# Performance work log

Hardware: AMD Instinct MI355X
Metric: run time of the kernel (lower is better)

Reference implementation:

```python
import jax, jax.numpy as jnp
import numpy as np

KH, KW = 3, 3
STRIDE = (1, 1)
PAD = ((1, 1), (1, 1))
WEIGHT_BIT = 8


def asym_quant_params(num_bits, smin, smax):
    # ZeroQ asymmetric_linear_quantization_params (signed, integral zero point)
    n = 2.0 ** num_bits - 1.0
    scale = n / jnp.maximum(smax - smin, 1e-8)
    zero_point = jnp.round(scale * smin) + 2.0 ** (num_bits - 1)
    return scale, zero_point


def setup_inputs() -> dict:
    key = jax.random.key(0)
    k1, k2, k3 = jax.random.split(key, 3)
    x = jax.random.normal(k1, (16, 128, 56, 56), dtype=jnp.float32)
    weight = jax.random.normal(k2, (128, 128, 3, 3), dtype=jnp.float32) * 0.05
    bias = jax.random.normal(k3, (128,), dtype=jnp.float32) * 0.1
    return {"x": x, "weight": weight, "bias": bias, "activation_bit": 8}


def reference(x, weight, bias, activation_bit):
    B, C, H, W = x.shape
    Cout = weight.shape[0]

    # nn.functional.unfold(x, 3, stride=1, padding=1).transpose(1, 2)
    # conv_general_dilated_patches emits feature dim ordered (c, kh, kw),
    # matching torch unfold's channel-major layout.
    patches = jax.lax.conv_general_dilated_patches(
        x, filter_shape=(KH, KW), window_strides=STRIDE, padding=PAD)
    _, F, OH, OW = patches.shape          # F = C*KH*KW
    L = OH * OW
    calc_x = patches.reshape(B, F, L).transpose(0, 2, 1)  # [B, L, F]

    # ----- weight quantization: per-output-channel asymmetric int8 -----
    w2 = weight.reshape(Cout, -1)                          # [Cout, F]
    w_min = w2.min(axis=1)
    w_max = w2.max(axis=1)
    scale_w, zp_w = asym_quant_params(WEIGHT_BIT, w_min, w_max)  # [Cout]
    nw = 2.0 ** (WEIGHT_BIT - 1)
    qw = jnp.clip(jnp.round(scale_w[:, None] * w2 - zp_w[:, None]), -nw, nw - 1)

    # ----- activation quantization: per-tensor asymmetric -----
    x_min = calc_x.min()
    x_max = calc_x.max()
    scale_x, zp_x = asym_quant_params(activation_bit, x_min, x_max)
    nx = 2.0 ** (activation_bit - 1)
    qx = jnp.clip(jnp.round(scale_x * calc_x - zp_x), -nx, nx - 1)  # [B, L, F]

    # bias: linear_quantize(bias, scale_w*scale_x, 0)
    qb = jnp.round(scale_w * scale_x * bias)                # [Cout]

    # integer matmul + asymmetric zero-point correction
    # real value r ~= (q + zp) / scale, so
    # x.w*sx*sw = qx.qw + zp_w*sum(qx) + zp_x*sum(qw) + K*zp_w*zp_x
    mult_res = jnp.einsum('blf,of->blo', qx, qw)            # [B, L, Cout]
    K = w2.shape[1]
    res = (mult_res
           + zp_w * qx.sum(-1, keepdims=True)               # [B, L, 1]*[Cout]
           + zp_x * qw.sum(axis=1)                          # [Cout]
           + K * zp_w * zp_x
           + qb)                                            # [B, L, Cout]

    # requantize accumulator to activation_bit bits, then dequantize
    r_min, r_max = res.min(), res.max()
    scale_r, zp_r = asym_quant_params(activation_bit, r_min, r_max)
    nr = 2.0 ** (activation_bit - 1)
    qr = jnp.clip(jnp.round(scale_r * res - zp_r), -nr, nr - 1)
    out = (qr + zp_r) / scale_r / (scale_w * scale_x)       # [B, L, Cout]

    return out.transpose(0, 2, 1)                           # [B, Cout, L]
```

## Files before the change

### kernel.cpp

```cpp
#include <hip/hip_runtime.h>
#include <stdint.h>

#pragma clang fp contract(off)

typedef __attribute__((ext_vector_type(4))) int i32x4;
typedef __attribute__((ext_vector_type(16))) int i32x16;

#define B_    16
#define C_    128
#define HW_   56
#define L_    3136
#define CO_   128
#define F_    1152
#define M_    50176
#define NT_   784

#define OFF_PBMIN 0
#define OFF_PBMAX 3136
#define OFF_PRMIN 6272
#define OFF_PRMAX 9408
#define OFF_SW    12544
#define OFF_ZPW   13056
#define OFF_SXZX  13568
#define OFF_CNT   14080
#define OFF_QS    15616
#define OFF_QW    16384
#define OFF_QX    163840
#define OFF_S     6586368
#define OFF_RES   6787072

__device__ __forceinline__ int read_abit(const int* p) {
    int i = *p;
    if (i > 0 && i < 32) return i;
    float f = __int_as_float(i);
    int fi = (int)f;
    return (fi > 0 && fi < 32) ? fi : 8;
}

__device__ __forceinline__ int swz_tile(int blk) {
    return (blk & 7) * 98 + (blk >> 3);
}

__device__ __forceinline__ void gsync(char* ws, int sp) {
    unsigned* base = (unsigned*)(ws + OFF_CNT) + sp * 128;
    __syncthreads();
    if (threadIdx.x == 0) {
        __threadfence();
        atomicAdd(&base[(blockIdx.x & 7) * 16], 1u);
    }
    if (threadIdx.x < 8) {
        while (__hip_atomic_load(&base[threadIdx.x * 16],
                                 __ATOMIC_RELAXED, __HIP_MEMORY_SCOPE_AGENT) < 98u)
            __builtin_amdgcn_s_sleep(2);
    }
    __threadfence();
    __syncthreads();
}

__device__ __forceinline__ void block_fminmax(float& mn, float& mx, float* sred) {
    for (int m = 32; m; m >>= 1) {
        mn = fminf(mn, __shfl_xor(mn, m));
        mx = fmaxf(mx, __shfl_xor(mx, m));
    }
    int w = threadIdx.x >> 6;
    if ((threadIdx.x & 63) == 0) { sred[w] = mn; sred[4 + w] = mx; }
    __syncthreads();
    mn = fminf(fminf(sred[0], sred[1]), fminf(sred[2], sred[3]));
    mx = fmaxf(fmaxf(sred[4], sred[5]), fmaxf(sred[6], sred[7]));
    __syncthreads();
}
__device__ __forceinline__ void block_iminmax(int& mn, int& mx, int* ired) {
    for (int m = 32; m; m >>= 1) {
        mn = min(mn, __shfl_xor(mn, m));
        mx = max(mx, __shfl_xor(mx, m));
    }
    int w = threadIdx.x >> 6;
    if ((threadIdx.x & 63) == 0) { ired[w] = mn; ired[4 + w] = mx; }
    __syncthreads();
    mn = min(min(ired[0], ired[1]), min(ired[2], ired[3]));
    mx = max(max(ired[4], ired[5]), max(ired[6], ired[7]));
    __syncthreads();
}
__device__ __forceinline__ int block_isum(int v, int* ired) {
    for (int m = 32; m; m >>= 1) v += __shfl_xor(v, m);
    int w = threadIdx.x >> 6;
    if ((threadIdx.x & 63) == 0) ired[w] = v;
    __syncthreads();
    v = ired[0] + ired[1] + ired[2] + ired[3];
    __syncthreads();
    return v;
}

__global__ __launch_bounds__(256) void kA1(const float4* __restrict__ x4,
                                           char* __restrict__ ws) {
    __shared__ float sred[8];
    float mn = 0.0f, mx = 0.0f;
    int base = blockIdx.x * blockDim.x + threadIdx.x;
    int stride = NT_ * 256;
    #pragma unroll
    for (int k = 0; k < 8; ++k) {
        float4 v = x4[base + k * stride];
        mn = fminf(mn, fminf(fminf(v.x, v.y), fminf(v.z, v.w)));
        mx = fmaxf(mx, fmaxf(fmaxf(v.x, v.y), fmaxf(v.z, v.w)));
    }
    block_fminmax(mn, mx, sred);
    if (threadIdx.x == 0) {
        ((float*)(ws + OFF_PBMIN))[blockIdx.x] = mn;
        ((float*)(ws + OFF_PBMAX))[blockIdx.x] = mx;
    }
}

__global__ __launch_bounds__(256) void kA2(const float* __restrict__ wgt,
                                           const int* __restrict__ abit_p,
                                           char* __restrict__ ws) {
    __shared__ float sred[8];
    __shared__ int ired[8];
    if (blockIdx.x == CO_) {
        const float* pbmin = (const float*)(ws + OFF_PBMIN);
        const float* pbmax = (const float*)(ws + OFF_PBMAX);
        float mn = 0.0f, mx = 0.0f;
        for (int i = threadIdx.x; i < NT_; i += 256) {
            mn = fminf(mn, pbmin[i]);
            mx = fmaxf(mx, pbmax[i]);
        }
        block_fminmax(mn, mx, sred);
        if (threadIdx.x == 0) {
            int abit = read_abit(abit_p);
            float nlv = (float)((1 << abit) - 1);
            float sx = nlv / fmaxf(mx - mn, 1e-8f);
            float zx = rintf(sx * mn) + (float)(1 << (abit - 1));
            ((float*)(ws + OFF_SXZX))[0] = sx;
            ((float*)(ws + OFF_SXZX))[1] = zx;
        }
        return;
    }
    int o = blockIdx.x;
    const float* wr = wgt + o * F_;
    float mn = 3.4e38f, mx = -3.4e38f;
    for (int f = threadIdx.x; f < F_; f += 256) {
        float v = wr[f];
        mn = fminf(mn, v); mx = fmaxf(mx, v);
    }
    block_fminmax(mn, mx, sred);
    float sw = 255.0f / fmaxf(mx - mn, 1e-8f);
    float zw = rintf(sw * mn) + 128.0f;
    signed char* qw = (signed char*)(ws + OFF_QW);
    int qsum = 0;
    for (int f = threadIdx.x; f < F_; f += 256) {
        float q = fminf(fmaxf(rintf(sw * wr[f] - zw), -128.0f), 127.0f);
        int qi = (int)q;
        qsum += qi;
        int c = f / 9, j = f - c * 9;
        qw[j * 16384 + (c >> 4) * 2048 + (o << 4) + (c & 15)] = (signed char)qi;
    }
    qsum = block_isum(qsum, ired);
    if (threadIdx.x == 0) {
        ((int*)(ws + OFF_QS))[o]  = qsum;
        ((int*)(ws + OFF_ZPW))[o] = (int)zw;
        ((float*)(ws + OFF_SW))[o] = sw;
    }
}

__device__ __forceinline__ void dev_p2x(const float* __restrict__ x, char* ws, char* pool,
                                        float sx, float zx, int nx) {
    int (*ssum)[64] = (int(*)[64])pool;
    float lo = -(float)nx, hif = (float)(nx - 1);
    signed char* qxt = (signed char*)(ws + OFF_QX);
    int gid = swz_tile(blockIdx.x);
    int b = gid / 49, lcq = gid - b * 49;
    int l0 = lcq * 64;
    int t = threadIdx.x, lane = t & 63, cgp = t >> 6;
    int l = l0 + lane;
    const float* xb = x + ((size_t)b * C_) * L_ + l;
    int4* dst = (int4*)(qxt + ((size_t)(b * L_ + l)) * 128);
    int psum = 0;
    #pragma unroll
    for (int ii = 0; ii < 2; ++ii) {
        int c16 = (cgp + 4 * ii) * 16;
        int wds[4];
        #pragma unroll
        for (int k = 0; k < 4; ++k) {
            int wv = 0;
            #pragma unroll
            for (int e = 0; e < 4; ++e) {
                int c = c16 + 4 * k + e;
                float v = xb[(size_t)c * L_];
                int qi = (int)fminf(fmaxf(rintf(sx * v - zx), lo), hif);
                psum += qi;
                wv |= (qi & 255) << (8 * e);
            }
            wds[k] = wv;
        }
        int4 vv; vv.x = wds[0]; vv.y = wds[1]; vv.z = wds[2]; vv.w = wds[3];
        dst[c16 >> 4] = vv;
    }
    ssum[cgp][lane] = psum;
    __syncthreads();
    if (cgp == 0) {
        int* S = (int*)(ws + OFF_S);
        S[b * L_ + l] = ssum[0][lane] + ssum[1][lane] + ssum[2][lane] + ssum[3][lane];
    }
    __syncthreads();
}

template <bool WRITE_RES>
__device__ __forceinline__ void dev_p3(char* __restrict__ ws, char* pool, int* ired,
                                       const float* __restrict__ bias,
                                       int abit, float sx, float zx,
                                       i32x16& acc0, i32x16& acc1) {
    signed char* As = (signed char*)pool;
    signed char* Bs = (signed char*)(pool + 8192);
    int* S_s = (int*)(pool + 24576);
    int* sq  = (int*)(pool + 25504);
    const signed char* qxt = (const signed char*)(ws + OFF_QX);
    const signed char* qw  = (const signed char*)(ws + OFF_QW);
    const int* Sg  = (const int*)(ws + OFF_S);
    const int* zpw = (const int*)(ws + OFF_ZPW);

    int t = threadIdx.x;
    int mg = swz_tile(blockIdx.x) * 64;
    int b = mg / L_, l0 = mg - b * L_;
    int prow0 = l0 / HW_;
    int nx = 1 << (abit - 1);
    int q0 = min(max(-(int)zx, -nx), nx - 1);
    int pw = (q0 & 255) * 0x01010101;
    int4 pad4; pad4.x = pw; pad4.y = pw; pad4.z = pw; pad4.w = pw;
    int padS = C_ * q0;
    const signed char* qxtb = qxt + (size_t)b * L_ * 128;
    const int* Sb = Sg + b * L_;

    int chA = t & 7, rowA0 = t >> 3, rowA1 = rowA0 + 32;
    int li0 = l0 + rowA0, li1 = l0 + rowA1;
    int oh0 = li0 / HW_, ow0 = li0 - oh0 * HW_;
    int oh1 = li1 / HW_, ow1 = li1 - oh1 * HW_;

    int4 a0, a1, br0, br1, br2, br3;
    #define P3_LOAD_A(J) do {                                                          \
        int kh = (J) / 3 - 1, kw = (J) % 3 - 1;                                        \
        int ih = oh0 + kh, iw = ow0 + kw;                                              \
        a0 = ((unsigned)ih < HW_ && (unsigned)iw < HW_)                                \
             ? *(const int4*)(qxtb + ((ih * HW_ + iw) << 7) + (chA << 4)) : pad4;      \
        ih = oh1 + kh; iw = ow1 + kw;                                                  \
        a1 = ((unsigned)ih < HW_ && (unsigned)iw < HW_)                                \
             ? *(const int4*)(qxtb + ((ih * HW_ + iw) << 7) + (chA << 4)) : pad4;      \
    } while (0)
    #define P3_LOAD_B(J) do {                                                          \
        const int4* src = (const int4*)(qw + (J) * 16384);                             \
        br0 = src[t]; br1 = src[256 + t]; br2 = src[512 + t]; br3 = src[768 + t];      \
    } while (0)

    P3_LOAD_A(0); P3_LOAD_B(0);
    if (t < 232) {
        int ri = t / 58, c1 = t - ri * 58;
        int ih = prow0 - 1 + ri, iw = c1 - 1;
        S_s[t] = ((unsigned)ih < HW_ && (unsigned)iw < HW_) ? Sb[ih * HW_ + iw] : padS;
    }
    __syncthreads();
    if (t < 64) {
        int l = l0 + t;
        int oh = l / HW_, ow = l - oh * HW_;
        int ri = oh - prow0 + 1, ci = ow + 1;
        int s = 0;
        #pragma unroll
        for (int dr = -1; dr <= 1; ++dr)
            #pragma unroll
            for (int dc = -1; dc <= 1; ++dc)
                s += S_s[(ri + dr) * 58 + ci + dc];
        sq[t] = s;
    }

    int lane = t & 63, w = t >> 6;
    int wm = (w >> 1) << 5, wn = (w & 1) << 6;
    int r = lane & 31, hi = lane >> 5;
    #pragma unroll
    for (int i = 0; i < 16; ++i) { acc0[i] = 0; acc1[i] = 0; }

    #pragma unroll
    for (int j = 0; j < 9; ++j) {
        if (j > 0) __syncthreads();
        *(int4*)&As[(rowA0 << 7) + ((chA ^ (rowA0 & 7)) << 4)] = a0;
        *(int4*)&As[(rowA1 << 7) + ((chA ^ (rowA1 & 7)) << 4)] = a1;
        {
            int4* d = (int4*)Bs;
            d[t] = br0; d[256 + t] = br1; d[512 + t] = br2; d[768 + t] = br3;
        }
        if (j < 8) { P3_LOAD_A(j + 1); P3_LOAD_B(j + 1); }
        __syncthreads();
        i32x4 af[4], bf0[4], bf1[4];
        #pragma unroll
        for (int kk = 0; kk < 4; ++kk) {
            int ch2 = kk * 2 + hi, row = wm + r;
            af[kk]  = *(const i32x4*)&As[(row << 7) + ((ch2 ^ (row & 7)) << 4)];
            bf0[kk] = *(const i32x4*)&Bs[ch2 * 2048 + ((wn + r) << 4)];
            bf1[kk] = *(const i32x4*)&Bs[ch2 * 2048 + ((wn + 32 + r) << 4)];
        }
        #pragma unroll
        for (int kk = 0; kk < 4; ++kk) {
            acc0 = __builtin_amdgcn_mfma_i32_32x32x32_i8(af[kk], bf0[kk], acc0, 0, 0, 0);
            acc1 = __builtin_amdgcn_mfma_i32_32x32x32_i8(af[kk], bf1[kk], acc1, 0, 0, 0);
        }
    }
    #undef P3_LOAD_A
    #undef P3_LOAD_B

    int o0 = wn + r, o1 = wn + 32 + r;
    const int* qs = (const int*)(ws + OFF_QS);
    const float* swp = (const float*)(ws + OFF_SW);
    int zxi = (int)zx;
    int zw0 = zpw[o0], zw1 = zpw[o1];
    int c0 = zxi * qs[o0] + F_ * zw0 * zxi + (int)rintf(swp[o0] * sx * bias[o0]);
    int c1 = zxi * qs[o1] + F_ * zw1 * zxi + (int)rintf(swp[o1] * sx * bias[o1]);
    int lmin = INT32_MAX, lmax = INT32_MIN;
    int* resp = (int*)(ws + OFF_RES);
    #pragma unroll
    for (int g = 0; g < 16; ++g) {
        int row = wm + (g & 3) + ((g >> 2) << 3) + (hi << 2);
        int s = sq[row];
        int v0 = acc0[g] + zw0 * s + c0;
        int v1 = acc1[g] + zw1 * s + c1;
        acc0[g] = v0; acc1[g] = v1;
        lmin = min(lmin, min(v0, v1));
        lmax = max(lmax, max(v0, v1));
        if (WRITE_RES) {
            int m = mg + row;
            resp[m * CO_ + o0] = v0;
            resp[m * CO_ + o1] = v1;
        }
    }
    block_iminmax(lmin, lmax, ired);
    if (t == 0) {
        ((int*)(ws + OFF_PRMIN))[blockIdx.x] = lmin;
        ((int*)(ws + OFF_PRMAX))[blockIdx.x] = lmax;
    }
    __syncthreads();
}

__device__ __forceinline__ void dev_reduce_pr(const char* ws, int* ired,
                                              int& rmin, int& rmax) {
    const int* prmin = (const int*)(ws + OFF_PRMIN);
    const int* prmax = (const int*)(ws + OFF_PRMAX);
    int mn = INT32_MAX, mx = INT32_MIN;
    for (int i = threadIdx.x; i < NT_; i += 256) {
        mn = min(mn, prmin[i]);
        mx = max(mx, prmax[i]);
    }
    block_iminmax(mn, mx, ired);
    rmin = mn; rmax = mx;
}

__device__ __forceinline__ void dev_p4(const char* ws, char* pool, float* __restrict__ out,
                                       int abit, float sx, int rmin, int rmax,
                                       const i32x16& acc0, const i32x16& acc1) {
    const float* scale_w = (const float*)(ws + OFF_SW);
    float* tile = (float*)pool;
    int t = threadIdx.x;
    int mg = swz_tile(blockIdx.x) * 64;
    int b = mg / L_, l0 = mg - b * L_;
    int lane = t & 63, w = t >> 6;
    int wm = (w >> 1) << 5, wn = (w & 1) << 6;
    int r = lane & 31, hi = lane >> 5;
    int o0 = wn + r, o1 = wn + 32 + r;
    int nx = 1 << (abit - 1);
    float nlev = (float)((1 << abit) - 1);
    float rminf = (float)rmin, rmaxf = (float)rmax;
    float sr = nlev / fmaxf(rmaxf - rminf, 1e-8f);
    float zr = rintf(sr * rminf) + (float)nx;
    float lo = -(float)nx, hiq = (float)(nx - 1);
    float swsx0 = scale_w[o0] * sx, swsx1 = scale_w[o1] * sx;
    #pragma unroll
    for (int g = 0; g < 16; ++g) {
        int row = wm + (g & 3) + ((g >> 2) << 3) + (hi << 2);
        float qa = fminf(fmaxf(rintf(sr * (float)acc0[g] - zr), lo), hiq);
        float qb = fminf(fmaxf(rintf(sr * (float)acc1[g] - zr), lo), hiq);
        tile[row * 129 + o0] = ((qa + zr) / sr) / swsx0;
        tile[row * 129 + o1] = ((qb + zr) / sr) / swsx1;
    }
    __syncthreads();
    #pragma unroll
    for (int i = 0; i < 8; ++i) {
        int o = (t >> 4) + i * 16;
        int l4 = (t & 15) * 4;
        float4 f;
        #pragma unroll
        for (int jj = 0; jj < 4; ++jj)
            ((float*)&f)[jj] = tile[(l4 + jj) * 129 + o];
        *(float4*)(out + ((size_t)(b * CO_ + o)) * L_ + l0 + l4) = f;
    }
}

__global__ __launch_bounds__(256, 4) void kB(const float* __restrict__ x,
                                             const float* __restrict__ bias,
                                             const int* __restrict__ abit_p,
                                             char* __restrict__ ws,
                                             float* __restrict__ out) {
    __shared__ __align__(16) char pool[33280];
    __shared__ int ired[8];

    float sx = ((const float*)(ws + OFF_SXZX))[0];
    float zx = ((const float*)(ws + OFF_SXZX))[1];
    int abit = read_abit(abit_p);
    int nx = 1 << (abit - 1);

    dev_p2x(x, ws, pool, sx, zx, nx);
    gsync(ws, 0);

    i32x16 acc0, acc1;
    dev_p3<false>(ws, pool, ired, bias, abit, sx, zx, acc0, acc1);
    gsync(ws, 1);

    int rmin, rmax;
    dev_reduce_pr(ws, ired, rmin, rmax);
    dev_p4(ws, pool, out, abit, sx, rmin, rmax, acc0, acc1);
}

__global__ __launch_bounds__(256) void fbB1(const float* __restrict__ x,
                                            const int* __restrict__ abit_p,
                                            char* __restrict__ ws) {
    __shared__ __align__(16) char pool[1024];
    float sx = ((const float*)(ws + OFF_SXZX))[0];
    float zx = ((const float*)(ws + OFF_SXZX))[1];
    int abit = read_abit(abit_p);
    int nx = 1 << (abit - 1);
    dev_p2x(x, ws, pool, sx, zx, nx);
}

__global__ __launch_bounds__(256, 4) void fbB2(const float* __restrict__ bias,
                                               const int* __restrict__ abit_p,
                                               char* __restrict__ ws) {
    __shared__ __align__(16) char pool[25760];
    __shared__ int ired[8];
    float sx = ((const float*)(ws + OFF_SXZX))[0];
    float zx = ((const float*)(ws + OFF_SXZX))[1];
    int abit = read_abit(abit_p);
    i32x16 acc0, acc1;
    dev_p3<true>(ws, pool, ired, bias, abit, sx, zx, acc0, acc1);
}

__global__ __launch_bounds__(256) void fbB3(const int* __restrict__ abit_p,
                                            char* __restrict__ ws,
                                            float* __restrict__ out) {
    __shared__ int tile[64 * 65];
    __shared__ int ired[8];
    float sxv = ((const float*)(ws + OFF_SXZX))[0];
    int abit = read_abit(abit_p);
    float nlv = (float)((1 << abit) - 1);
    int rmin, rmax;
    dev_reduce_pr(ws, ired, rmin, rmax);

    const int* res = (const int*)(ws + OFF_RES);
    const float* scale_w = (const float*)(ws + OFF_SW);
    int t = threadIdx.x;
    int bid = blockIdx.x;
    int lcq = bid % 49; int tmp2 = bid / 49; int ocq = tmp2 & 1; int b = tmp2 >> 1;
    int l0 = lcq * 64, o0 = ocq * 64;

    const int* resb = res + ((size_t)(b * L_ + l0)) * CO_ + o0;
    #pragma unroll
    for (int i = 0; i < 4; ++i) {
        int lr = (t >> 4) + i * 16;
        int oc4 = (t & 15) * 4;
        int4 v = *(const int4*)(resb + lr * CO_ + oc4);
        int* d = &tile[lr * 65 + oc4];
        d[0] = v.x; d[1] = v.y; d[2] = v.z; d[3] = v.w;
    }
    int nxq = 1 << (abit - 1);
    float rminf = (float)rmin, rmaxf = (float)rmax;
    float sr = nlv / fmaxf(rmaxf - rminf, 1e-8f);
    float zr = rintf(sr * rminf) + (float)nxq;
    float lo = -(float)nxq, hiq = (float)(nxq - 1);
    __syncthreads();
    #pragma unroll
    for (int i = 0; i < 4; ++i) {
        int o = (t >> 4) + i * 16;
        int l4 = (t & 15) * 4;
        float swsx = scale_w[o0 + o] * sxv;
        float4 f;
        #pragma unroll
        for (int jj = 0; jj < 4; ++jj) {
            int rv = tile[(l4 + jj) * 65 + o];
            float q = fminf(fmaxf(rintf(sr * (float)rv - zr), lo), hiq);
            ((float*)&f)[jj] = ((q + zr) / sr) / swsx;
        }
        *(float4*)(out + ((size_t)(b * CO_ + o0 + o)) * L_ + l0 + l4) = f;
    }
}


extern "C" void kernel_launch(void* const* d_in, const int* in_sizes, int n_in,
                              void* d_out, int out_size, void* d_ws, size_t ws_size,
                              hipStream_t stream) {
    const float* x      = (const float*)d_in[0];
    const float* weight = (const float*)d_in[1];
    const float* bias   = (const float*)d_in[2];
    const int*   abit   = (const int*)d_in[3];
    float* out = (float*)d_out;
    char* ws = (char*)d_ws;

    int dev = 0;
    hipGetDevice(&dev);
    int ncu = 0;
    hipDeviceGetAttribute(&ncu, hipDeviceAttributeMultiprocessorCount, dev);
    int nb = 0;
    hipOccupancyMaxActiveBlocksPerMultiprocessor(&nb, (const void*)kB, 256, 0);

    kA1<<<NT_, 256, 0, stream>>>((const float4*)x, ws);
    kA2<<<CO_ + 1, 256, 0, stream>>>(weight, abit, ws);

    if (nb > 0 && (long)nb * (long)ncu >= NT_) {
        hipMemsetAsync(ws + OFF_CNT, 0, 1024, stream);
        kB<<<NT_, 256, 0, stream>>>(x, bias, abit, ws, out);
    } else {
        fbB1<<<NT_, 256, 0, stream>>>(x, abit, ws);
        fbB2<<<NT_, 256, 0, stream>>>(bias, abit, ws);
        fbB3<<<1568, 256, 0, stream>>>(abit, ws, out);
    }
}
```

Measured before the change: 54.63 us.

## Fuse activation quantization into conv GEMM via in-LDS halo tile, drop one grid sync

Removes the separate quantize-and-store pass for activations. Each block now loads a 4-row input halo straight from x, quantizes it into a swizzled LDS buffer, and computes the row sums locally. The tile grows to 112 output pixels (two image rows) with four MFMA accumulators per wave, and weight tiles are double-buffered so each tap needs only one barrier. The grid drops to 448 blocks with one global barrier instead of two, cutting the int8 activation round trip through global memory. In exchange, blocks use more LDS and registers with lower occupancy, halo rows are re-quantized by neighbouring blocks, and some lanes go partly idle on the 112-row tile.

```diff
diff --git a/kernel.cpp b/kernel.cpp
--- a/kernel.cpp
+++ b/kernel.cpp
@@ -13,21 +13,24 @@
 #define CO_   128
 #define F_    1152
 #define M_    50176
-#define NT_   784
-
-#define OFF_PBMIN 0
-#define OFF_PBMAX 3136
-#define OFF_PRMIN 6272
-#define OFF_PRMAX 9408
-#define OFF_SW    12544
-#define OFF_ZPW   13056
-#define OFF_SXZX  13568
-#define OFF_CNT   14080
-#define OFF_QS    15616
+#define NT1_  784
+#define NTC_  448
+
+#define OFF_PRMIN 0
+#define OFF_PRMAX 2048
+#define OFF_PBMIN 4096
+#define OFF_PBMAX 8192
+#define OFF_SW    12288
+#define OFF_ZPW   12800
+#define OFF_SXZX  13312
+#define OFF_CNT   13440
+#define OFF_QS    14080
 #define OFF_QW    16384
-#define OFF_QX    163840
-#define OFF_S     6586368
-#define OFF_RES   6787072
+#define OFF_RES   163840
+
+#define HALO_B 29696
+#define BS_B   16384
+#define POOL_B (HALO_B + 2 * BS_B)
 
 __device__ __forceinline__ int read_abit(const int* p) {
     int i = *p;
@@ -38,11 +41,11 @@
 }
 
 __device__ __forceinline__ int swz_tile(int blk) {
-    return (blk & 7) * 98 + (blk >> 3);
-}
-
-__device__ __forceinline__ void gsync(char* ws, int sp) {
-    unsigned* base = (unsigned*)(ws + OFF_CNT) + sp * 128;
+    return (blk & 7) * 56 + (blk >> 3);
+}
+
+__device__ __forceinline__ void gsync(char* ws) {
+    unsigned* base = (unsigned*)(ws + OFF_CNT);
     __syncthreads();
     if (threadIdx.x == 0) {
         __threadfence();
@@ -50,7 +53,7 @@
     }
     if (threadIdx.x < 8) {
         while (__hip_atomic_load(&base[threadIdx.x * 16],
-                                 __ATOMIC_RELAXED, __HIP_MEMORY_SCOPE_AGENT) < 98u)
+                                 __ATOMIC_RELAXED, __HIP_MEMORY_SCOPE_AGENT) < 56u)
             __builtin_amdgcn_s_sleep(2);
     }
     __threadfence();
@@ -96,7 +99,7 @@
     __shared__ float sred[8];
     float mn = 0.0f, mx = 0.0f;
     int base = blockIdx.x * blockDim.x + threadIdx.x;
-    int stride = NT_ * 256;
+    int stride = NT1_ * 256;
     #pragma unroll
     for (int k = 0; k < 8; ++k) {
         float4 v = x4[base + k * stride];
@@ -119,7 +122,7 @@
         const float* pbmin = (const float*)(ws + OFF_PBMIN);
         const float* pbmax = (const float*)(ws + OFF_PBMAX);
         float mn = 0.0f, mx = 0.0f;
-        for (int i = threadIdx.x; i < NT_; i += 256) {
+        for (int i = threadIdx.x; i < NT1_; i += 256) {
             mn = fminf(mn, pbmin[i]);
             mx = fmaxf(mx, pbmax[i]);
         }
@@ -161,103 +164,92 @@
     }
 }
 
-__device__ __forceinline__ void dev_p2x(const float* __restrict__ x, char* ws, char* pool,
-                                        float sx, float zx, int nx) {
-    int (*ssum)[64] = (int(*)[64])pool;
-    float lo = -(float)nx, hif = (float)(nx - 1);
-    signed char* qxt = (signed char*)(ws + OFF_QX);
-    int gid = swz_tile(blockIdx.x);
-    int b = gid / 49, lcq = gid - b * 49;
-    int l0 = lcq * 64;
-    int t = threadIdx.x, lane = t & 63, cgp = t >> 6;
-    int l = l0 + lane;
-    const float* xb = x + ((size_t)b * C_) * L_ + l;
-    int4* dst = (int4*)(qxt + ((size_t)(b * L_ + l)) * 128);
-    int psum = 0;
-    #pragma unroll
-    for (int ii = 0; ii < 2; ++ii) {
-        int c16 = (cgp + 4 * ii) * 16;
-        int wds[4];
-        #pragma unroll
-        for (int k = 0; k < 4; ++k) {
-            int wv = 0;
-            #pragma unroll
-            for (int e = 0; e < 4; ++e) {
-                int c = c16 + 4 * k + e;
-                float v = xb[(size_t)c * L_];
-                int qi = (int)fminf(fmaxf(rintf(sx * v - zx), lo), hif);
-                psum += qi;
-                wv |= (qi & 255) << (8 * e);
-            }
-            wds[k] = wv;
-        }
-        int4 vv; vv.x = wds[0]; vv.y = wds[1]; vv.z = wds[2]; vv.w = wds[3];
-        dst[c16 >> 4] = vv;
-    }
-    ssum[cgp][lane] = psum;
-    __syncthreads();
-    if (cgp == 0) {
-        int* S = (int*)(ws + OFF_S);
-        S[b * L_ + l] = ssum[0][lane] + ssum[1][lane] + ssum[2][lane] + ssum[3][lane];
-    }
-    __syncthreads();
-}
-
 template <bool WRITE_RES>
-__device__ __forceinline__ void dev_p3(char* __restrict__ ws, char* pool, int* ired,
-                                       const float* __restrict__ bias,
-                                       int abit, float sx, float zx,
-                                       i32x16& acc0, i32x16& acc1) {
-    signed char* As = (signed char*)pool;
-    signed char* Bs = (signed char*)(pool + 8192);
-    int* S_s = (int*)(pool + 24576);
-    int* sq  = (int*)(pool + 25504);
-    const signed char* qxt = (const signed char*)(ws + OFF_QX);
-    const signed char* qw  = (const signed char*)(ws + OFF_QW);
-    const int* Sg  = (const int*)(ws + OFF_S);
+__device__ __forceinline__ void dev_main(const float* __restrict__ x,
+                                         const float* __restrict__ bias,
+                                         char* __restrict__ ws, char* pool,
+                                         int* S_s, int* sq, int* ired,
+                                         int abit, float sx, float zx,
+                                         i32x16& a00, i32x16& a01,
+                                         i32x16& a10, i32x16& a11,
+                                         int& mgout) {
+    signed char* NB  = (signed char*)pool;
+    signed char* Bs0 = (signed char*)(pool + HALO_B);
+    signed char* Bs1 = Bs0 + BS_B;
+    const signed char* qw = (const signed char*)(ws + OFF_QW);
     const int* zpw = (const int*)(ws + OFF_ZPW);
 
     int t = threadIdx.x;
-    int mg = swz_tile(blockIdx.x) * 64;
+    int mg = swz_tile(blockIdx.x) * 112;
+    mgout = mg;
     int b = mg / L_, l0 = mg - b * L_;
     int prow0 = l0 / HW_;
     int nx = 1 << (abit - 1);
     int q0 = min(max(-(int)zx, -nx), nx - 1);
     int pw = (q0 & 255) * 0x01010101;
     int4 pad4; pad4.x = pw; pad4.y = pw; pad4.z = pw; pad4.w = pw;
-    int padS = C_ * q0;
-    const signed char* qxtb = qxt + (size_t)b * L_ * 128;
-    const int* Sb = Sg + b * L_;
-
-    int chA = t & 7, rowA0 = t >> 3, rowA1 = rowA0 + 32;
-    int li0 = l0 + rowA0, li1 = l0 + rowA1;
-    int oh0 = li0 / HW_, ow0 = li0 - oh0 * HW_;
-    int oh1 = li1 / HW_, ow1 = li1 - oh1 * HW_;
-
-    int4 a0, a1, br0, br1, br2, br3;
-    #define P3_LOAD_A(J) do {                                                          \
-        int kh = (J) / 3 - 1, kw = (J) % 3 - 1;                                        \
-        int ih = oh0 + kh, iw = ow0 + kw;                                              \
-        a0 = ((unsigned)ih < HW_ && (unsigned)iw < HW_)                                \
-             ? *(const int4*)(qxtb + ((ih * HW_ + iw) << 7) + (chA << 4)) : pad4;      \
-        ih = oh1 + kh; iw = ow1 + kw;                                                  \
-        a1 = ((unsigned)ih < HW_ && (unsigned)iw < HW_)                                \
-             ? *(const int4*)(qxtb + ((ih * HW_ + iw) << 7) + (chA << 4)) : pad4;      \
-    } while (0)
-    #define P3_LOAD_B(J) do {                                                          \
-        const int4* src = (const int4*)(qw + (J) * 16384);                             \
-        br0 = src[t]; br1 = src[256 + t]; br2 = src[512 + t]; br3 = src[768 + t];      \
-    } while (0)
-
-    P3_LOAD_A(0); P3_LOAD_B(0);
+    const float* xb = x + (size_t)b * C_ * L_;
+
+    int4 br0, br1, br2, br3;
+    {
+        const int4* src = (const int4*)qw;
+        br0 = src[t]; br1 = src[256 + t]; br2 = src[512 + t]; br3 = src[768 + t];
+    }
+
+    #pragma unroll
+    for (int i = 0; i < 8; ++i) {
+        int s = t + i * 256;
+        if (s < 1856) ((int4*)NB)[s] = pad4;
+    }
+    __syncthreads();
+
+    {
+        float lo = -(float)nx, hif = (float)(nx - 1);
+        #pragma unroll
+        for (int i = 0; i < 28; ++i) {
+            int u = t + i * 256;
+            int c = u / 56, rem = u - c * 56;
+            int ri = rem / 14, f4 = rem - ri * 14;
+            int ih = prow0 - 1 + ri;
+            if ((unsigned)ih < HW_) {
+                float4 v = *(const float4*)(xb + (size_t)c * L_ + ih * HW_ + f4 * 4);
+                int ch = c >> 4, byte = c & 15;
+                #pragma unroll
+                for (int k = 0; k < 4; ++k) {
+                    float xv = ((const float*)&v)[k];
+                    int qi = (int)fminf(fmaxf(rintf(sx * xv - zx), lo), hif);
+                    int pix = ri * 58 + f4 * 4 + k + 1;
+                    NB[(pix << 7) + ((ch ^ (pix & 7)) << 4) + byte] = (signed char)qi;
+                }
+            }
+        }
+    }
+    {
+        int4* d = (int4*)Bs0;
+        d[t] = br0; d[256 + t] = br1; d[512 + t] = br2; d[768 + t] = br3;
+        const int4* src = (const int4*)(qw + BS_B);
+        br0 = src[t]; br1 = src[256 + t]; br2 = src[512 + t]; br3 = src[768 + t];
+    }
+    __syncthreads();
+
     if (t < 232) {
-        int ri = t / 58, c1 = t - ri * 58;
-        int ih = prow0 - 1 + ri, iw = c1 - 1;
-        S_s[t] = ((unsigned)ih < HW_ && (unsigned)iw < HW_) ? Sb[ih * HW_ + iw] : padS;
-    }
-    __syncthreads();
-    if (t < 64) {
-        int l = l0 + t;
+        int s = 0;
+        #pragma unroll
+        for (int ch = 0; ch < 8; ++ch) {
+            int4 v = *(const int4*)&NB[(t << 7) + ((ch ^ (t & 7)) << 4)];
+            #pragma unroll
+            for (int k2 = 0; k2 < 4; ++k2) {
+                int wv = ((const int*)&v)[k2];
+                s += (int)(signed char)wv + (int)(signed char)(wv >> 8)
+                   + (int)(signed char)(wv >> 16) + (int)(signed char)(wv >> 24);
+            }
+        }
+        S_s[t] = s;
+    }
+    __syncthreads();
+    if (t < 128) {
+        int rl = min(t, 111);
+        int l = l0 + rl;
         int oh = l / HW_, ow = l - oh * HW_;
         int ri = oh - prow0 + 1, ci = ow + 1;
         int s = 0;
@@ -270,38 +262,57 @@
     }
 
     int lane = t & 63, w = t >> 6;
-    int wm = (w >> 1) << 5, wn = (w & 1) << 6;
+    int wm = (w >> 1) << 6;
+    int wn = (w & 1) << 6;
     int r = lane & 31, hi = lane >> 5;
-    #pragma unroll
-    for (int i = 0; i < 16; ++i) { acc0[i] = 0; acc1[i] = 0; }
+
+    int pb0, pb1;
+    {
+        int l = l0 + wm + r;
+        int oh = l / HW_, ow = l - oh * HW_;
+        pb0 = (oh - prow0 + 1) * 58 + ow + 1;
+    }
+    {
+        int rl = min(wm + 32 + r, 111);
+        int l = l0 + rl;
+        int oh = l / HW_, ow = l - oh * HW_;
+        pb1 = (oh - prow0 + 1) * 58 + ow + 1;
+    }
+
+    #pragma unroll
+    for (int i = 0; i < 16; ++i) { a00[i] = 0; a01[i] = 0; a10[i] = 0; a11[i] = 0; }
 
     #pragma unroll
     for (int j = 0; j < 9; ++j) {
-        if (j > 0) __syncthreads();
-        *(int4*)&As[(rowA0 << 7) + ((chA ^ (rowA0 & 7)) << 4)] = a0;
-        *(int4*)&As[(rowA1 << 7) + ((chA ^ (rowA1 & 7)) << 4)] = a1;
-        {
-            int4* d = (int4*)Bs;
+        if (j < 8) {
+            int4* d = (int4*)(((j + 1) & 1) ? Bs1 : Bs0);
             d[t] = br0; d[256 + t] = br1; d[512 + t] = br2; d[768 + t] = br3;
-        }
-        if (j < 8) { P3_LOAD_A(j + 1); P3_LOAD_B(j + 1); }
+            if (j < 7) {
+                const int4* src = (const int4*)(qw + (j + 2) * BS_B);
+                br0 = src[t]; br1 = src[256 + t]; br2 = src[512 + t]; br3 = src[768 + t];
+            }
+        }
+        const signed char* Bc = (j & 1) ? Bs1 : Bs0;
+        int dj = (j / 3 - 1) * 58 + (j % 3 - 1);
+        i32x4 af0[4], af1[4], bf0[4], bf1[4];
+        #pragma unroll
+        for (int kk = 0; kk < 4; ++kk) {
+            int ch2 = kk * 2 + hi;
+            int p0 = pb0 + dj, p1 = pb1 + dj;
+            af0[kk] = *(const i32x4*)&NB[(p0 << 7) + ((ch2 ^ (p0 & 7)) << 4)];
+            af1[kk] = *(const i32x4*)&NB[(p1 << 7) + ((ch2 ^ (p1 & 7)) << 4)];
+            bf0[kk] = *(const i32x4*)&Bc[ch2 * 2048 + ((wn + r) << 4)];
+            bf1[kk] = *(const i32x4*)&Bc[ch2 * 2048 + ((wn + 32 + r) << 4)];
+        }
+        #pragma unroll
+        for (int kk = 0; kk < 4; ++kk) {
+            a00 = __builtin_amdgcn_mfma_i32_32x32x32_i8(af0[kk], bf0[kk], a00, 0, 0, 0);
+            a01 = __builtin_amdgcn_mfma_i32_32x32x32_i8(af0[kk], bf1[kk], a01, 0, 0, 0);
+            a10 = __builtin_amdgcn_mfma_i32_32x32x32_i8(af1[kk], bf0[kk], a10, 0, 0, 0);
+            a11 = __builtin_amdgcn_mfma_i32_32x32x32_i8(af1[kk], bf1[kk], a11, 0, 0, 0);
+        }
         __syncthreads();
-        i32x4 af[4], bf0[4], bf1[4];
-        #pragma unroll
-        for (int kk = 0; kk < 4; ++kk) {
-            int ch2 = kk * 2 + hi, row = wm + r;
-            af[kk]  = *(const i32x4*)&As[(row << 7) + ((ch2 ^ (row & 7)) << 4)];
-            bf0[kk] = *(const i32x4*)&Bs[ch2 * 2048 + ((wn + r) << 4)];
-            bf1[kk] = *(const i32x4*)&Bs[ch2 * 2048 + ((wn + 32 + r) << 4)];
-        }
-        #pragma unroll
-        for (int kk = 0; kk < 4; ++kk) {
-            acc0 = __builtin_amdgcn_mfma_i32_32x32x32_i8(af[kk], bf0[kk], acc0, 0, 0, 0);
-            acc1 = __builtin_amdgcn_mfma_i32_32x32x32_i8(af[kk], bf1[kk], acc1, 0, 0, 0);
-        }
-    }
-    #undef P3_LOAD_A
-    #undef P3_LOAD_B
+    }
 
     int o0 = wn + r, o1 = wn + 32 + r;
     const int* qs = (const int*)(ws + OFF_QS);
@@ -314,17 +325,27 @@
     int* resp = (int*)(ws + OFF_RES);
     #pragma unroll
     for (int g = 0; g < 16; ++g) {
-        int row = wm + (g & 3) + ((g >> 2) << 3) + (hi << 2);
-        int s = sq[row];
-        int v0 = acc0[g] + zw0 * s + c0;
-        int v1 = acc1[g] + zw1 * s + c1;
-        acc0[g] = v0; acc1[g] = v1;
-        lmin = min(lmin, min(v0, v1));
-        lmax = max(lmax, max(v0, v1));
+        int sub = (g & 3) + ((g >> 2) << 3) + (hi << 2);
+        int r0 = wm + sub, r1 = wm + 32 + sub;
+        int s0 = sq[r0], s1 = sq[r1];
+        int v00 = a00[g] + zw0 * s0 + c0;
+        int v01 = a01[g] + zw1 * s0 + c1;
+        int v10 = a10[g] + zw0 * s1 + c0;
+        int v11 = a11[g] + zw1 * s1 + c1;
+        a00[g] = v00; a01[g] = v01; a10[g] = v10; a11[g] = v11;
+        lmin = min(lmin, min(v00, v01));
+        lmax = max(lmax, max(v00, v01));
+        if (r1 < 112) {
+            lmin = min(lmin, min(v10, v11));
+            lmax = max(lmax, max(v10, v11));
+        }
         if (WRITE_RES) {
-            int m = mg + row;
-            resp[m * CO_ + o0] = v0;
-            resp[m * CO_ + o1] = v1;
+            resp[(mg + r0) * CO_ + o0] = v00;
+            resp[(mg + r0) * CO_ + o1] = v01;
+            if (r1 < 112) {
+                resp[(mg + r1) * CO_ + o0] = v10;
+                resp[(mg + r1) * CO_ + o1] = v11;
+            }
         }
     }
     block_iminmax(lmin, lmax, ired);
@@ -340,7 +361,7 @@
     const int* prmin = (const int*)(ws + OFF_PRMIN);
     const int* prmax = (const int*)(ws + OFF_PRMAX);
     int mn = INT32_MAX, mx = INT32_MIN;
-    for (int i = threadIdx.x; i < NT_; i += 256) {
+    for (int i = threadIdx.x; i < NTC_; i += 256) {
         mn = min(mn, prmin[i]);
         mx = max(mx, prmax[i]);
     }
@@ -348,97 +369,98 @@
     rmin = mn; rmax = mx;
 }
 
-__device__ __forceinline__ void dev_p4(const char* ws, char* pool, float* __restrict__ out,
-                                       int abit, float sx, int rmin, int rmax,
-                                       const i32x16& acc0, const i32x16& acc1) {
-    const float* scale_w = (const float*)(ws + OFF_SW);
-    float* tile = (float*)pool;
+__global__ __launch_bounds__(256, 2) void kC(const float* __restrict__ x,
+                                             const float* __restrict__ bias,
+                                             const int* __restrict__ abit_p,
+                                             char* __restrict__ ws,
+                                             float* __restrict__ out) {
+    __shared__ __align__(16) char pool[POOL_B];
+    __shared__ int S_s[232];
+    __shared__ int sq[128];
+    __shared__ int ired[8];
+
+    float sx = ((const float*)(ws + OFF_SXZX))[0];
+    float zx = ((const float*)(ws + OFF_SXZX))[1];
+    int abit = read_abit(abit_p);
+
+    i32x16 a00, a01, a10, a11;
+    int mg;
+    dev_main<false>(x, bias, ws, pool, S_s, sq, ired, abit, sx, zx,
+                    a00, a01, a10, a11, mg);
+    gsync(ws);
+
+    int rmin, rmax;
+    dev_reduce_pr(ws, ired, rmin, rmax);
+
+    const float* swp = (const float*)(ws + OFF_SW);
     int t = threadIdx.x;
-    int mg = swz_tile(blockIdx.x) * 64;
     int b = mg / L_, l0 = mg - b * L_;
     int lane = t & 63, w = t >> 6;
-    int wm = (w >> 1) << 5, wn = (w & 1) << 6;
+    int wm = (w >> 1) << 6, wn = (w & 1) << 6;
     int r = lane & 31, hi = lane >> 5;
     int o0 = wn + r, o1 = wn + 32 + r;
     int nx = 1 << (abit - 1);
     float nlev = (float)((1 << abit) - 1);
-    float rminf = (float)rmin, rmaxf = (float)rmax;
-    float sr = nlev / fmaxf(rmaxf - rminf, 1e-8f);
-    float zr = rintf(sr * rminf) + (float)nx;
+    float sr = nlev / fmaxf((float)rmax - (float)rmin, 1e-8f);
+    float zr = rintf(sr * (float)rmin) + (float)nx;
     float lo = -(float)nx, hiq = (float)(nx - 1);
-    float swsx0 = scale_w[o0] * sx, swsx1 = scale_w[o1] * sx;
-    #pragma unroll
-    for (int g = 0; g < 16; ++g) {
-        int row = wm + (g & 3) + ((g >> 2) << 3) + (hi << 2);
-        float qa = fminf(fmaxf(rintf(sr * (float)acc0[g] - zr), lo), hiq);
-        float qb = fminf(fmaxf(rintf(sr * (float)acc1[g] - zr), lo), hiq);
-        tile[row * 129 + o0] = ((qa + zr) / sr) / swsx0;
-        tile[row * 129 + o1] = ((qb + zr) / sr) / swsx1;
-    }
-    __syncthreads();
-    #pragma unroll
-    for (int i = 0; i < 8; ++i) {
-        int o = (t >> 4) + i * 16;
-        int l4 = (t & 15) * 4;
-        float4 f;
-        #pragma unroll
-        for (int jj = 0; jj < 4; ++jj)
-            ((float*)&f)[jj] = tile[(l4 + jj) * 129 + o];
-        *(float4*)(out + ((size_t)(b * CO_ + o)) * L_ + l0 + l4) = f;
-    }
-}
-
-__global__ __launch_bounds__(256, 4) void kB(const float* __restrict__ x,
-                                             const float* __restrict__ bias,
-                                             const int* __restrict__ abit_p,
-                                             char* __restrict__ ws,
-                                             float* __restrict__ out) {
-    __shared__ __align__(16) char pool[33280];
-    __shared__ int ired[8];
-
-    float sx = ((const float*)(ws + OFF_SXZX))[0];
-    float zx = ((const float*)(ws + OFF_SXZX))[1];
-    int abit = read_abit(abit_p);
-    int nx = 1 << (abit - 1);
-
-    dev_p2x(x, ws, pool, sx, zx, nx);
-    gsync(ws, 0);
-
-    i32x16 acc0, acc1;
-    dev_p3<false>(ws, pool, ired, bias, abit, sx, zx, acc0, acc1);
-    gsync(ws, 1);
-
-    int rmin, rmax;
-    dev_reduce_pr(ws, ired, rmin, rmax);
-    dev_p4(ws, pool, out, abit, sx, rmin, rmax, acc0, acc1);
-}
-
-__global__ __launch_bounds__(256) void fbB1(const float* __restrict__ x,
-                                            const int* __restrict__ abit_p,
-                                            char* __restrict__ ws) {
-    __shared__ __align__(16) char pool[1024];
-    float sx = ((const float*)(ws + OFF_SXZX))[0];
-    float zx = ((const float*)(ws + OFF_SXZX))[1];
-    int abit = read_abit(abit_p);
-    int nx = 1 << (abit - 1);
-    dev_p2x(x, ws, pool, sx, zx, nx);
-}
-
-__global__ __launch_bounds__(256, 4) void fbB2(const float* __restrict__ bias,
-                                               const int* __restrict__ abit_p,
-                                               char* __restrict__ ws) {
-    __shared__ __align__(16) char pool[25760];
+    float swsx0 = swp[o0] * sx, swsx1 = swp[o1] * sx;
+    float* tile = (float*)pool;
+
+    #pragma unroll
+    for (int rid = 0; rid < 2; ++rid) {
+        __syncthreads();
+        if (wm == rid * 64) {
+            #pragma unroll
+            for (int g = 0; g < 16; ++g) {
+                int sub = (g & 3) + ((g >> 2) << 3) + (hi << 2);
+                float qa = fminf(fmaxf(rintf(sr * (float)a00[g] - zr), lo), hiq);
+                float qb = fminf(fmaxf(rintf(sr * (float)a01[g] - zr), lo), hiq);
+                float qc = fminf(fmaxf(rintf(sr * (float)a10[g] - zr), lo), hiq);
+                float qd = fminf(fmaxf(rintf(sr * (float)a11[g] - zr), lo), hiq);
+                tile[sub * 129 + o0] = ((qa + zr) / sr) / swsx0;
+                tile[sub * 129 + o1] = ((qb + zr) / sr) / swsx1;
+                tile[(32 + sub) * 129 + o0] = ((qc + zr) / sr) / swsx0;
+                tile[(32 + sub) * 129 + o1] = ((qd + zr) / sr) / swsx1;
+            }
+        }
+        __syncthreads();
+        int nrows = (rid == 0) ? 64 : 48;
+        #pragma unroll
+        for (int i = 0; i < 8; ++i) {
+            int o = (t >> 4) + i * 16;
+            int l4 = (t & 15) * 4;
+            if (l4 < nrows) {
+                float4 f;
+                #pragma unroll
+                for (int jj = 0; jj < 4; ++jj)
+                    ((float*)&f)[jj] = tile[(l4 + jj) * 129 + o];
+                *(float4*)(out + ((size_t)(b * CO_ + o)) * L_ + l0 + rid * 64 + l4) = f;
+            }
+        }
+    }
+}
+
+__global__ __launch_bounds__(256, 2) void fbC(const float* __restrict__ x,
+                                              const float* __restrict__ bias,
+                                              const int* __restrict__ abit_p,
+                                              char* __restrict__ ws) {
+    __shared__ __align__(16) char pool[POOL_B];
+    __shared__ int S_s[232];
+    __shared__ int sq[128];
     __shared__ int ired[8];
     float sx = ((const float*)(ws + OFF_SXZX))[0];
     float zx = ((const float*)(ws + OFF_SXZX))[1];
     int abit = read_abit(abit_p);
-    i32x16 acc0, acc1;
-    dev_p3<true>(ws, pool, ired, bias, abit, sx, zx, acc0, acc1);
-}
-
-__global__ __launch_bounds__(256) void fbB3(const int* __restrict__ abit_p,
-                                            char* __restrict__ ws,
-                                            float* __restrict__ out) {
+    i32x16 a00, a01, a10, a11;
+    int mg;
+    dev_main<true>(x, bias, ws, pool, S_s, sq, ired, abit, sx, zx,
+                   a00, a01, a10, a11, mg);
+}
+
+__global__ __launch_bounds__(256) void fbD(const int* __restrict__ abit_p,
+                                           char* __restrict__ ws,
+                                           float* __restrict__ out) {
     __shared__ int tile[64 * 65];
     __shared__ int ired[8];
     float sxv = ((const float*)(ws + OFF_SXZX))[0];
@@ -464,9 +486,8 @@
         d[0] = v.x; d[1] = v.y; d[2] = v.z; d[3] = v.w;
     }
     int nxq = 1 << (abit - 1);
-    float rminf = (float)rmin, rmaxf = (float)rmax;
-    float sr = nlv / fmaxf(rmaxf - rminf, 1e-8f);
-    float zr = rintf(sr * rminf) + (float)nxq;
+    float sr = nlv / fmaxf((float)rmax - (float)rmin, 1e-8f);
+    float zr = rintf(sr * (float)rmin) + (float)nxq;
     float lo = -(float)nxq, hiq = (float)(nxq - 1);
     __syncthreads();
     #pragma unroll
@@ -501,17 +522,16 @@
     int ncu = 0;
     hipDeviceGetAttribute(&ncu, hipDeviceAttributeMultiprocessorCount, dev);
     int nb = 0;
-    hipOccupancyMaxActiveBlocksPerMultiprocessor(&nb, (const void*)kB, 256, 0);
-
-    kA1<<<NT_, 256, 0, stream>>>((const float4*)x, ws);
+    hipOccupancyMaxActiveBlocksPerMultiprocessor(&nb, (const void*)kC, 256, 0);
+
+    kA1<<<NT1_, 256, 0, stream>>>((const float4*)x, ws);
     kA2<<<CO_ + 1, 256, 0, stream>>>(weight, abit, ws);
 
-    if (nb > 0 && (long)nb * (long)ncu >= NT_) {
-        hipMemsetAsync(ws + OFF_CNT, 0, 1024, stream);
-        kB<<<NT_, 256, 0, stream>>>(x, bias, abit, ws, out);
+    if (nb > 0 && (long)nb * (long)ncu >= NTC_) {
+        hipMemsetAsync(ws + OFF_CNT, 0, 512, stream);
+        kC<<<NTC_, 256, 0, stream>>>(x, bias, abit, ws, out);
     } else {
-        fbB1<<<NT_, 256, 0, stream>>>(x, abit, ws);
-        fbB2<<<NT_, 256, 0, stream>>>(bias, abit, ws);
-        fbB3<<<1568, 256, 0, stream>>>(abit, ws, out);
-    }
-}
+        fbC<<<NTC_, 256, 0, stream>>>(x, bias, abit, ws);
+        fbD<<<1568, 256, 0, stream>>>(abit, ws, out);
+    }
+}
```

Measured after the change: 95.19 us. 74.2% more time.

## Replace persistent grid-synced kernel with three separate kernel launches

Applied to the files above, without the earlier changes.

Removes the cooperative single-kernel path, which used software grid barriers via atomic counters and kept accumulators in registers across phases. The work is now always split into three kernels: quantize/pack activations, integer GEMM that writes the full int32 result to workspace, and a dequantize kernel that reads it back. This drops the spin-wait barriers, the counter memset and the host-side occupancy queries. In exchange it adds a global write and read of the int32 result tensor and two extra kernel launches.

```diff
diff --git a/kernel.cpp b/kernel.cpp
--- a/kernel.cpp
+++ b/kernel.cpp
@@ -16,18 +16,17 @@
 #define NT_   784
 
 #define OFF_PBMIN 0
-#define OFF_PBMAX 3136
-#define OFF_PRMIN 6272
-#define OFF_PRMAX 9408
-#define OFF_SW    12544
-#define OFF_ZPW   13056
-#define OFF_SXZX  13568
-#define OFF_CNT   14080
-#define OFF_QS    15616
-#define OFF_QW    16384
-#define OFF_QX    163840
-#define OFF_S     6586368
-#define OFF_RES   6787072
+#define OFF_PBMAX 4096
+#define OFF_PRMIN 8192
+#define OFF_PRMAX 12288
+#define OFF_SW    16384
+#define OFF_ZPW   16896
+#define OFF_SXZX  17408
+#define OFF_QS    17536
+#define OFF_QW    18432
+#define OFF_QX    165888
+#define OFF_S     6588416
+#define OFF_RES   6789120
 
 __device__ __forceinline__ int read_abit(const int* p) {
     int i = *p;
@@ -39,22 +38,6 @@
 
 __device__ __forceinline__ int swz_tile(int blk) {
     return (blk & 7) * 98 + (blk >> 3);
-}
-
-__device__ __forceinline__ void gsync(char* ws, int sp) {
-    unsigned* base = (unsigned*)(ws + OFF_CNT) + sp * 128;
-    __syncthreads();
-    if (threadIdx.x == 0) {
-        __threadfence();
-        atomicAdd(&base[(blockIdx.x & 7) * 16], 1u);
-    }
-    if (threadIdx.x < 8) {
-        while (__hip_atomic_load(&base[threadIdx.x * 16],
-                                 __ATOMIC_RELAXED, __HIP_MEMORY_SCOPE_AGENT) < 98u)
-            __builtin_amdgcn_s_sleep(2);
-    }
-    __threadfence();
-    __syncthreads();
 }
 
 __device__ __forceinline__ void block_fminmax(float& mn, float& mx, float* sred) {
@@ -161,9 +144,14 @@
     }
 }
 
-__device__ __forceinline__ void dev_p2x(const float* __restrict__ x, char* ws, char* pool,
-                                        float sx, float zx, int nx) {
-    int (*ssum)[64] = (int(*)[64])pool;
+__global__ __launch_bounds__(256) void kP2x(const float* __restrict__ x,
+                                            const int* __restrict__ abit_p,
+                                            char* __restrict__ ws) {
+    __shared__ int ssum[4][64];
+    float sx = ((const float*)(ws + OFF_SXZX))[0];
+    float zx = ((const float*)(ws + OFF_SXZX))[1];
+    int abit = read_abit(abit_p);
+    int nx = 1 << (abit - 1);
     float lo = -(float)nx, hif = (float)(nx - 1);
     signed char* qxt = (signed char*)(ws + OFF_QX);
     int gid = swz_tile(blockIdx.x);
@@ -200,14 +188,14 @@
         int* S = (int*)(ws + OFF_S);
         S[b * L_ + l] = ssum[0][lane] + ssum[1][lane] + ssum[2][lane] + ssum[3][lane];
     }
-    __syncthreads();
-}
-
-template <bool WRITE_RES>
-__device__ __forceinline__ void dev_p3(char* __restrict__ ws, char* pool, int* ired,
-                                       const float* __restrict__ bias,
-                                       int abit, float sx, float zx,
-                                       i32x16& acc0, i32x16& acc1) {
+}
+
+__global__ __launch_bounds__(256, 4) void kGEMM(const float* __restrict__ bias,
+                                                const int* __restrict__ abit_p,
+                                                char* __restrict__ ws) {
+    __shared__ __align__(16) char pool[25760];
+    __shared__ int ired[8];
+
     signed char* As = (signed char*)pool;
     signed char* Bs = (signed char*)(pool + 8192);
     int* S_s = (int*)(pool + 24576);
@@ -216,6 +204,10 @@
     const signed char* qw  = (const signed char*)(ws + OFF_QW);
     const int* Sg  = (const int*)(ws + OFF_S);
     const int* zpw = (const int*)(ws + OFF_ZPW);
+
+    float sx = ((const float*)(ws + OFF_SXZX))[0];
+    float zx = ((const float*)(ws + OFF_SXZX))[1];
+    int abit = read_abit(abit_p);
 
     int t = threadIdx.x;
     int mg = swz_tile(blockIdx.x) * 64;
@@ -272,6 +264,7 @@
     int lane = t & 63, w = t >> 6;
     int wm = (w >> 1) << 5, wn = (w & 1) << 6;
     int r = lane & 31, hi = lane >> 5;
+    i32x16 acc0, acc1;
     #pragma unroll
     for (int i = 0; i < 16; ++i) { acc0[i] = 0; acc1[i] = 0; }
 
@@ -318,125 +311,20 @@
         int s = sq[row];
         int v0 = acc0[g] + zw0 * s + c0;
         int v1 = acc1[g] + zw1 * s + c1;
-        acc0[g] = v0; acc1[g] = v1;
         lmin = min(lmin, min(v0, v1));
         lmax = max(lmax, max(v0, v1));
-        if (WRITE_RES) {
-            int m = mg + row;
-            resp[m * CO_ + o0] = v0;
-            resp[m * CO_ + o1] = v1;
-        }
+        int m = mg + row;
+        resp[m * CO_ + o0] = v0;
+        resp[m * CO_ + o1] = v1;
     }
     block_iminmax(lmin, lmax, ired);
     if (t == 0) {
         ((int*)(ws + OFF_PRMIN))[blockIdx.x] = lmin;
         ((int*)(ws + OFF_PRMAX))[blockIdx.x] = lmax;
     }
-    __syncthreads();
-}
-
-__device__ __forceinline__ void dev_reduce_pr(const char* ws, int* ired,
-                                              int& rmin, int& rmax) {
-    const int* prmin = (const int*)(ws + OFF_PRMIN);
-    const int* prmax = (const int*)(ws + OFF_PRMAX);
-    int mn = INT32_MAX, mx = INT32_MIN;
-    for (int i = threadIdx.x; i < NT_; i += 256) {
-        mn = min(mn, prmin[i]);
-        mx = max(mx, prmax[i]);
-    }
-    block_iminmax(mn, mx, ired);
-    rmin = mn; rmax = mx;
-}
-
-__device__ __forceinline__ void dev_p4(const char* ws, char* pool, float* __restrict__ out,
-                                       int abit, float sx, int rmin, int rmax,
-                                       const i32x16& acc0, const i32x16& acc1) {
-    const float* scale_w = (const float*)(ws + OFF_SW);
-    float* tile = (float*)pool;
-    int t = threadIdx.x;
-    int mg = swz_tile(blockIdx.x) * 64;
-    int b = mg / L_, l0 = mg - b * L_;
-    int lane = t & 63, w = t >> 6;
-    int wm = (w >> 1) << 5, wn = (w & 1) << 6;
-    int r = lane & 31, hi = lane >> 5;
-    int o0 = wn + r, o1 = wn + 32 + r;
-    int nx = 1 << (abit - 1);
-    float nlev = (float)((1 << abit) - 1);
-    float rminf = (float)rmin, rmaxf = (float)rmax;
-    float sr = nlev / fmaxf(rmaxf - rminf, 1e-8f);
-    float zr = rintf(sr * rminf) + (float)nx;
-    float lo = -(float)nx, hiq = (float)(nx - 1);
-    float swsx0 = scale_w[o0] * sx, swsx1 = scale_w[o1] * sx;
-    #pragma unroll
-    for (int g = 0; g < 16; ++g) {
-        int row = wm + (g & 3) + ((g >> 2) << 3) + (hi << 2);
-        float qa = fminf(fmaxf(rintf(sr * (float)acc0[g] - zr), lo), hiq);
-        float qb = fminf(fmaxf(rintf(sr * (float)acc1[g] - zr), lo), hiq);
-        tile[row * 129 + o0] = ((qa + zr) / sr) / swsx0;
-        tile[row * 129 + o1] = ((qb + zr) / sr) / swsx1;
-    }
-    __syncthreads();
-    #pragma unroll
-    for (int i = 0; i < 8; ++i) {
-        int o = (t >> 4) + i * 16;
-        int l4 = (t & 15) * 4;
-        float4 f;
-        #pragma unroll
-        for (int jj = 0; jj < 4; ++jj)
-            ((float*)&f)[jj] = tile[(l4 + jj) * 129 + o];
-        *(float4*)(out + ((size_t)(b * CO_ + o)) * L_ + l0 + l4) = f;
-    }
-}
-
-__global__ __launch_bounds__(256, 4) void kB(const float* __restrict__ x,
-                                             const float* __restrict__ bias,
-                                             const int* __restrict__ abit_p,
-                                             char* __restrict__ ws,
-                                             float* __restrict__ out) {
-    __shared__ __align__(16) char pool[33280];
-    __shared__ int ired[8];
-
-    float sx = ((const float*)(ws + OFF_SXZX))[0];
-    float zx = ((const float*)(ws + OFF_SXZX))[1];
-    int abit = read_abit(abit_p);
-    int nx = 1 << (abit - 1);
-
-    dev_p2x(x, ws, pool, sx, zx, nx);
-    gsync(ws, 0);
-
-    i32x16 acc0, acc1;
-    dev_p3<false>(ws, pool, ired, bias, abit, sx, zx, acc0, acc1);
-    gsync(ws, 1);
-
-    int rmin, rmax;
-    dev_reduce_pr(ws, ired, rmin, rmax);
-    dev_p4(ws, pool, out, abit, sx, rmin, rmax, acc0, acc1);
-}
-
-__global__ __launch_bounds__(256) void fbB1(const float* __restrict__ x,
-                                            const int* __restrict__ abit_p,
-                                            char* __restrict__ ws) {
-    __shared__ __align__(16) char pool[1024];
-    float sx = ((const float*)(ws + OFF_SXZX))[0];
-    float zx = ((const float*)(ws + OFF_SXZX))[1];
-    int abit = read_abit(abit_p);
-    int nx = 1 << (abit - 1);
-    dev_p2x(x, ws, pool, sx, zx, nx);
-}
-
-__global__ __launch_bounds__(256, 4) void fbB2(const float* __restrict__ bias,
-                                               const int* __restrict__ abit_p,
-                                               char* __restrict__ ws) {
-    __shared__ __align__(16) char pool[25760];
-    __shared__ int ired[8];
-    float sx = ((const float*)(ws + OFF_SXZX))[0];
-    float zx = ((const float*)(ws + OFF_SXZX))[1];
-    int abit = read_abit(abit_p);
-    i32x16 acc0, acc1;
-    dev_p3<true>(ws, pool, ired, bias, abit, sx, zx, acc0, acc1);
-}
-
-__global__ __launch_bounds__(256) void fbB3(const int* __restrict__ abit_p,
+}
+
+__global__ __launch_bounds__(256) void kDEQ(const int* __restrict__ abit_p,
                                             char* __restrict__ ws,
                                             float* __restrict__ out) {
     __shared__ int tile[64 * 65];
@@ -444,8 +332,15 @@
     float sxv = ((const float*)(ws + OFF_SXZX))[0];
     int abit = read_abit(abit_p);
     float nlv = (float)((1 << abit) - 1);
-    int rmin, rmax;
-    dev_reduce_pr(ws, ired, rmin, rmax);
+
+    const int* prmin = (const int*)(ws + OFF_PRMIN);
+    const int* prmax = (const int*)(ws + OFF_PRMAX);
+    int rmin = INT32_MAX, rmax = INT32_MIN;
+    for (int i = threadIdx.x; i < NT_; i += 256) {
+        rmin = min(rmin, prmin[i]);
+        rmax = max(rmax, prmax[i]);
+    }
+    block_iminmax(rmin, rmax, ired);
 
     const int* res = (const int*)(ws + OFF_RES);
     const float* scale_w = (const float*)(ws + OFF_SW);
@@ -464,9 +359,8 @@
         d[0] = v.x; d[1] = v.y; d[2] = v.z; d[3] = v.w;
     }
     int nxq = 1 << (abit - 1);
-    float rminf = (float)rmin, rmaxf = (float)rmax;
-    float sr = nlv / fmaxf(rmaxf - rminf, 1e-8f);
-    float zr = rintf(sr * rminf) + (float)nxq;
+    float sr = nlv / fmaxf((float)rmax - (float)rmin, 1e-8f);
+    float zr = rintf(sr * (float)rmin) + (float)nxq;
     float lo = -(float)nxq, hiq = (float)(nxq - 1);
     __syncthreads();
     #pragma unroll
@@ -496,22 +390,9 @@
     float* out = (float*)d_out;
     char* ws = (char*)d_ws;
 
-    int dev = 0;
-    hipGetDevice(&dev);
-    int ncu = 0;
-    hipDeviceGetAttribute(&ncu, hipDeviceAttributeMultiprocessorCount, dev);
-    int nb = 0;
-    hipOccupancyMaxActiveBlocksPerMultiprocessor(&nb, (const void*)kB, 256, 0);
-
     kA1<<<NT_, 256, 0, stream>>>((const float4*)x, ws);
     kA2<<<CO_ + 1, 256, 0, stream>>>(weight, abit, ws);
-
-    if (nb > 0 && (long)nb * (long)ncu >= NT_) {
-        hipMemsetAsync(ws + OFF_CNT, 0, 1024, stream);
-        kB<<<NT_, 256, 0, stream>>>(x, bias, abit, ws, out);
-    } else {
-        fbB1<<<NT_, 256, 0, stream>>>(x, abit, ws);
-        fbB2<<<NT_, 256, 0, stream>>>(bias, abit, ws);
-        fbB3<<<1568, 256, 0, stream>>>(abit, ws, out);
-    }
-}
+    kP2x<<<NT_, 256, 0, stream>>>(x, abit, ws);
+    kGEMM<<<NT_, 256, 0, stream>>>(bias, abit, ws);
+    kDEQ<<<1568, 256, 0, stream>>>(abit, ws, out);
+}
```

After: 55.03 us. Within noise of the previous version (+0.7%).
